# Performance work log

Measured on AMD Instinct MI355X. Metric: run time of the kernel, lower is better.

The kernel has to match this reference:

```python
import jax, jax.numpy as jnp
import numpy as np

N_EMBD = 1024
N_HEAD = 16


def setup_inputs() -> dict:
    key = jax.random.key(0)
    ks = jax.random.split(key, 5)
    C = N_EMBD
    x = jax.random.normal(ks[0], (4, 2048, C), dtype=jnp.float32)
    s = 1.0 / np.sqrt(C)
    W_attn = jax.random.normal(ks[1], (C, 3 * C), dtype=jnp.float32) * s
    b_attn = jnp.zeros((3 * C,), dtype=jnp.float32)
    W_proj = jax.random.normal(ks[2], (C, C), dtype=jnp.float32) * s
    b_proj = jnp.zeros((C,), dtype=jnp.float32)
    return {"x": x, "W_attn": W_attn, "b_attn": b_attn, "W_proj": W_proj, "b_proj": b_proj}


def reference(x, W_attn, b_attn, W_proj, b_proj):
    B, T, C = x.shape
    H = N_HEAD
    D = C // H
    qkv = x @ W_attn + b_attn                      # [B,T,3C]
    q, k, v = jnp.split(qkv, 3, axis=-1)
    # [B,H,T,D]
    q = q.reshape(B, T, H, D).transpose(0, 2, 1, 3)
    k = k.reshape(B, T, H, D).transpose(0, 2, 1, 3)
    v = v.reshape(B, T, H, D).transpose(0, 2, 1, 3)
    scale = 1.0 / jnp.sqrt(jnp.asarray(D, dtype=x.dtype))
    att = jnp.einsum('bhqd,bhkd->bhqk', q, k) * scale   # [B,H,T,T]
    causal = jnp.tril(jnp.ones((T, T), dtype=bool))
    att = jnp.where(causal, att, jnp.finfo(att.dtype).min)
    att = jax.nn.softmax(att, axis=-1)
    y = jnp.einsum('bhqk,bhkd->bhqd', att, v)            # [B,H,T,D]
    y = y.transpose(0, 2, 1, 3).reshape(B, T, C)
    return y @ W_proj + b_proj
```

## Files before the change

### kernel.cpp

```cpp
#include <hip/hip_runtime.h>
#include <type_traits>

typedef __attribute__((ext_vector_type(8))) short short8;
typedef __attribute__((ext_vector_type(8))) unsigned short ushort8;
typedef __attribute__((ext_vector_type(4))) float floatx4;
typedef __attribute__((ext_vector_type(2))) unsigned int uintx2v;

__device__ __forceinline__ unsigned short f2bf(float f) {
    union { float f; unsigned int i; } v;
    v.f = f;
    unsigned int u = v.i;
    unsigned int r = (u + 0x7FFFu + ((u >> 16) & 1u)) >> 16;
    return (unsigned short)r;
}

__device__ __forceinline__ void gload_lds16(const unsigned short* g, unsigned short* lds_base) {
    __builtin_amdgcn_global_load_lds(
        (const __attribute__((address_space(1))) unsigned int*)g,
        (__attribute__((address_space(3))) unsigned int*)lds_base,
        16, 0, 0);
}

__device__ __forceinline__ void pbar() {
    asm volatile("" ::: "memory");
    __builtin_amdgcn_s_barrier();
    asm volatile("" ::: "memory");
}

__global__ __launch_bounds__(256) void cvt_f32_bf16_kernel(
    const float* __restrict__ src, unsigned short* __restrict__ dst, int n8)
{
    int i = blockIdx.x * 256 + threadIdx.x;
    if (i >= n8) return;
    const float4* s = (const float4*)src + (size_t)i * 2;
    float4 a = s[0];
    float4 b = s[1];
    ushort8 r;
    r[0] = f2bf(a.x); r[1] = f2bf(a.y); r[2] = f2bf(a.z); r[3] = f2bf(a.w);
    r[4] = f2bf(b.x); r[5] = f2bf(b.y); r[6] = f2bf(b.z); r[7] = f2bf(b.w);
    *((ushort8*)dst + i) = r;
}

__global__ __launch_bounds__(256) void transpose_cvt_kernel(
    const float* __restrict__ src, unsigned short* __restrict__ dst, int K, int N)
{
    __shared__ float tile[32][33];
    const int tx = threadIdx.x & 31;
    const int ty = threadIdx.x >> 5;
    const int k0 = blockIdx.y * 32, n0 = blockIdx.x * 32;
#pragma unroll
    for (int i = 0; i < 4; ++i)
        tile[ty + i * 8][tx] = src[(size_t)(k0 + ty + i * 8) * N + n0 + tx];
    __syncthreads();
#pragma unroll
    for (int i = 0; i < 4; ++i)
        dst[(size_t)(n0 + ty + i * 8) * K + k0 + tx] = f2bf(tile[tx][ty + i * 8]);
}

template <int MODE, typename OutT>
__global__ __launch_bounds__(256) void gemm128_kernel(
    const unsigned short* __restrict__ A,
    const unsigned short* __restrict__ Bt,
    const float* __restrict__ bias,
    OutT* __restrict__ C,
    unsigned short* __restrict__ Qo,
    unsigned short* __restrict__ Ko,
    unsigned short* __restrict__ Vto,
    int M, int N, int K)
{
    __shared__ __align__(16) unsigned short As[2][128 * 32];
    __shared__ __align__(16) unsigned short Bs[2][128 * 32];

    const int tid  = threadIdx.x;
    const int lane = tid & 63;
    const int w    = tid >> 6;
    const int wm   = w & 1;
    const int wn   = w >> 1;
    const int quad = lane >> 4;
    const int l16  = lane & 15;

    const int m0 = blockIdx.y * 128;
    const int n0 = blockIdx.x * 128;

    floatx4 acc[4][4];
#pragma unroll
    for (int i = 0; i < 4; ++i)
#pragma unroll
        for (int j = 0; j < 4; ++j) acc[i][j] = (floatx4)0.0f;

    const int r0 = tid >> 2;
    const int kc = (((tid & 3) ^ ((tid >> 3) & 3)) << 3);
    const unsigned short* Ag = A  + (size_t)(m0 + r0) * K + kc;
    const unsigned short* Bg = Bt + (size_t)(n0 + r0) * K + kc;

    const int sw = ((quad ^ ((l16 >> 1) & 3)) << 3);

    const int nt = K >> 5;

#define STAGE(buf, t)                                                          \
    do {                                                                       \
        const int kk = (t) << 5;                                               \
        gload_lds16(Ag + kk,                    &As[buf][w * 512]);            \
        gload_lds16(Ag + (size_t)64 * K + kk,   &As[buf][w * 512 + 2048]);     \
        gload_lds16(Bg + kk,                    &Bs[buf][w * 512]);            \
        gload_lds16(Bg + (size_t)64 * K + kk,   &Bs[buf][w * 512 + 2048]);     \
    } while (0)

    STAGE(0, 0);

    for (int t = 0; t < nt; ++t) {
        const int b = t & 1;
        if (t + 1 < nt) {
            STAGE(b ^ 1, t + 1);
            asm volatile("s_waitcnt vmcnt(4)" ::: "memory");
        } else {
            asm volatile("s_waitcnt vmcnt(0)" ::: "memory");
        }
        pbar();

        short8 a[4], bb[4];
#pragma unroll
        for (int mi = 0; mi < 4; ++mi)
            a[mi] = *(const short8*)&As[b][(wm * 64 + mi * 16 + l16) * 32 + sw];
#pragma unroll
        for (int ni = 0; ni < 4; ++ni)
            bb[ni] = *(const short8*)&Bs[b][(wn * 64 + ni * 16 + l16) * 32 + sw];
#pragma unroll
        for (int mi = 0; mi < 4; ++mi)
#pragma unroll
            for (int ni = 0; ni < 4; ++ni)
                acc[mi][ni] = __builtin_amdgcn_mfma_f32_16x16x32_bf16(a[mi], bb[ni], acc[mi][ni], 0, 0, 0);
        pbar();
    }
#undef STAGE

#pragma unroll
    for (int ni = 0; ni < 4; ++ni) {
        const int n = n0 + wn * 64 + ni * 16 + l16;
        const float bval = bias[n];
        const int seg = n >> 10;
        const int nl  = n & 1023;
#pragma unroll
        for (int mi = 0; mi < 4; ++mi) {
            if constexpr (MODE == 0) {
#pragma unroll
                for (int r = 0; r < 4; ++r) {
                    const int m = m0 + wm * 64 + mi * 16 + (quad << 2) + r;
                    const float val = acc[mi][ni][r] + bval;
                    if constexpr (std::is_same<OutT, unsigned short>::value)
                        C[(size_t)m * N + n] = f2bf(val);
                    else
                        C[(size_t)m * N + n] = val;
                }
            } else {
                if (seg < 2) {
                    unsigned short* P = (seg == 0) ? Qo : Ko;
#pragma unroll
                    for (int r = 0; r < 4; ++r) {
                        const int m = m0 + wm * 64 + mi * 16 + (quad << 2) + r;
                        P[(size_t)m * 1024 + nl] = f2bf(acc[mi][ni][r] + bval);
                    }
                } else {
                    const int mb = m0 + wm * 64 + mi * 16 + (quad << 2);
                    const int bbk = mb >> 11, t0 = mb & 2047;
                    unsigned int lo = (unsigned int)f2bf(acc[mi][ni][0] + bval) |
                                      ((unsigned int)f2bf(acc[mi][ni][1] + bval) << 16);
                    unsigned int hi = (unsigned int)f2bf(acc[mi][ni][2] + bval) |
                                      ((unsigned int)f2bf(acc[mi][ni][3] + bval) << 16);
                    uint2 pv; pv.x = lo; pv.y = hi;
                    *(uint2*)(Vto + ((size_t)bbk * 1024 + nl) * 2048 + t0) = pv;
                }
            }
        }
    }
}

__global__ __launch_bounds__(256, 6) void attn_kernel(
    const unsigned short* __restrict__ Q,
    const unsigned short* __restrict__ Kq,
    const unsigned short* __restrict__ Vt,
    unsigned short* __restrict__ Y)
{
    const int T = 2048;

    int idx = blockIdx.x;
    int qt  = 31 - (idx >> 6);
    int bh  = idx & 63;
    int b   = bh >> 4;
    int h   = bh & 15;

    const int tid  = threadIdx.x;
    const int lane = tid & 63;
    const int w    = tid >> 6;
    const int quad = lane >> 4;
    const int l16  = lane & 15;

    __shared__ __align__(16) unsigned short Ks2[8 * 64 * 8];
    __shared__ __align__(16) unsigned short Vs2[8 * 64 * 8];

    const unsigned short* qp =
        Q + (size_t)(b * T + qt * 64 + (w << 4) + l16) * 1024 + h * 64;
    short8 qf0 = *(const short8*)(qp + (quad << 3));
    short8 qf1 = *(const short8*)(qp + 32 + (quad << 3));

    float l_run = 0.0f;
    floatx4 o[4];
#pragma unroll
    for (int ns = 0; ns < 4; ++ns) o[ns] = (floatx4)0.0f;

    const unsigned short* kg0p = Kq + (size_t)(b * T + lane) * 1024 + h * 64 + (w) * 8;
    const unsigned short* kg1p = Kq + (size_t)(b * T + lane) * 1024 + h * 64 + (w + 4) * 8;
    const unsigned short* vg0p = Vt + ((size_t)(b * 1024 + h * 64 + lane)) * 2048 + (w) * 8;
    const unsigned short* vg1p = Vt + ((size_t)(b * 1024 + h * 64 + lane)) * 2048 + (w + 4) * 8;

    const int qg_local = (w << 4) + l16;

    const float SC2 = 0.18033688011112042f;
    const float MB2 = -17.312340490667562f;

    const int ktiles = qt + 1;
    for (int kt = 0; kt < ktiles; ++kt) {
        const int key0 = kt << 6;
        __syncthreads();
        gload_lds16(kg0p + (size_t)key0 * 1024, Ks2 + (w) * 512);
        gload_lds16(kg1p + (size_t)key0 * 1024, Ks2 + (w + 4) * 512);
        gload_lds16(vg0p + key0, Vs2 + (w) * 512);
        gload_lds16(vg1p + key0, Vs2 + (w + 4) * 512);
        __syncthreads();

        floatx4 s[4];
#pragma unroll
        for (int ks = 0; ks < 4; ++ks) {
            s[ks] = (floatx4)0.0f;
            short8 kf0 = *(const short8*)&Ks2[((0 * 4 + quad) * 64 + ks * 16 + l16) * 8];
            short8 kf1 = *(const short8*)&Ks2[((1 * 4 + quad) * 64 + ks * 16 + l16) * 8];
            s[ks] = __builtin_amdgcn_mfma_f32_16x16x32_bf16(kf0, qf0, s[ks], 0, 0, 0);
            s[ks] = __builtin_amdgcn_mfma_f32_16x16x32_bf16(kf1, qf1, s[ks], 0, 0, 0);
        }

        unsigned int plo[4], phi[4];
        if (kt < qt) {
#pragma unroll
            for (int ks = 0; ks < 4; ++ks) {
                float pv0 = __builtin_amdgcn_exp2f(fmaf(s[ks][0], SC2, MB2));
                float pv1 = __builtin_amdgcn_exp2f(fmaf(s[ks][1], SC2, MB2));
                float pv2 = __builtin_amdgcn_exp2f(fmaf(s[ks][2], SC2, MB2));
                float pv3 = __builtin_amdgcn_exp2f(fmaf(s[ks][3], SC2, MB2));
                l_run += (pv0 + pv1) + (pv2 + pv3);
                asm("v_cvt_pk_bf16_f32 %0, %1, %2" : "=v"(plo[ks]) : "v"(pv0), "v"(pv1));
                asm("v_cvt_pk_bf16_f32 %0, %1, %2" : "=v"(phi[ks]) : "v"(pv2), "v"(pv3));
            }
        } else {
            const int kq4 = quad << 2;
#pragma unroll
            for (int ks = 0; ks < 4; ++ks) {
                const int kb = (ks << 4) + kq4;
                float a0 = (kb + 0 <= qg_local) ? fmaf(s[ks][0], SC2, MB2) : -100000.0f;
                float a1 = (kb + 1 <= qg_local) ? fmaf(s[ks][1], SC2, MB2) : -100000.0f;
                float a2 = (kb + 2 <= qg_local) ? fmaf(s[ks][2], SC2, MB2) : -100000.0f;
                float a3 = (kb + 3 <= qg_local) ? fmaf(s[ks][3], SC2, MB2) : -100000.0f;
                float pv0 = __builtin_amdgcn_exp2f(a0);
                float pv1 = __builtin_amdgcn_exp2f(a1);
                float pv2 = __builtin_amdgcn_exp2f(a2);
                float pv3 = __builtin_amdgcn_exp2f(a3);
                l_run += (pv0 + pv1) + (pv2 + pv3);
                asm("v_cvt_pk_bf16_f32 %0, %1, %2" : "=v"(plo[ks]) : "v"(pv0), "v"(pv1));
                asm("v_cvt_pk_bf16_f32 %0, %1, %2" : "=v"(phi[ks]) : "v"(pv2), "v"(pv3));
            }
        }

        uintx2v t0 = __builtin_amdgcn_permlane32_swap(plo[0], plo[1], false, false);
        uintx2v u0 = __builtin_amdgcn_permlane16_swap(t0[0], t0[1], false, false);
        uintx2v t1 = __builtin_amdgcn_permlane32_swap(phi[0], phi[1], false, false);
        uintx2v u1 = __builtin_amdgcn_permlane16_swap(t1[0], t1[1], false, false);
        uintx2v t2 = __builtin_amdgcn_permlane32_swap(plo[2], plo[3], false, false);
        uintx2v u2 = __builtin_amdgcn_permlane16_swap(t2[0], t2[1], false, false);
        uintx2v t3 = __builtin_amdgcn_permlane32_swap(phi[2], phi[3], false, false);
        uintx2v u3 = __builtin_amdgcn_permlane16_swap(t3[0], t3[1], false, false);

        union { unsigned int d[4]; short8 v; } fa, fb;
        fa.d[0] = u0[0]; fa.d[1] = u1[0]; fa.d[2] = u0[1]; fa.d[3] = u1[1];
        fb.d[0] = u2[0]; fb.d[1] = u3[0]; fb.d[2] = u2[1]; fb.d[3] = u3[1];
        const short8 pf0 = fa.v;
        const short8 pf1 = fb.v;

#pragma unroll
        for (int ns = 0; ns < 4; ++ns) {
            short8 vf0 = *(const short8*)&Vs2[((0 * 4 + quad) * 64 + ns * 16 + l16) * 8];
            short8 vf1 = *(const short8*)&Vs2[((1 * 4 + quad) * 64 + ns * 16 + l16) * 8];
            o[ns] = __builtin_amdgcn_mfma_f32_16x16x32_bf16(pf0, vf0, o[ns], 0, 0, 0);
            o[ns] = __builtin_amdgcn_mfma_f32_16x16x32_bf16(pf1, vf1, o[ns], 0, 0, 0);
        }
    }

    float ssum = l_run;
    ssum += __shfl_xor(ssum, 16, 64);
    ssum += __shfl_xor(ssum, 32, 64);
    const float linv = 1.0f / ssum;
    float li[4];
#pragma unroll
    for (int r = 0; r < 4; ++r) li[r] = __shfl(linv, (quad << 2) + r, 64);

#pragma unroll
    for (int ns = 0; ns < 4; ++ns) {
        int d = (ns << 4) + l16;
#pragma unroll
        for (int r = 0; r < 4; ++r) {
            int t = qt * 64 + (w << 4) + (quad << 2) + r;
            Y[(size_t)(b * T + t) * 1024 + h * 64 + d] = f2bf(o[ns][r] * li[r]);
        }
    }
}

extern "C" void kernel_launch(void* const* d_in, const int* in_sizes, int n_in,
                              void* d_out, int out_size, void* d_ws, size_t ws_size,
                              hipStream_t stream) {
    const float* x  = (const float*)d_in[0];
    const float* Wa = (const float*)d_in[1];
    const float* ba = (const float*)d_in[2];
    const float* Wp = (const float*)d_in[3];
    const float* bp = (const float*)d_in[4];
    float* out = (float*)d_out;

    const size_t NX = (size_t)8192 * 1024;

    unsigned short* Qb  = (unsigned short*)d_ws;
    unsigned short* Kb  = Qb  + NX;
    unsigned short* Vtb = Kb  + NX;
    unsigned short* Yb  = Vtb + NX;
    unsigned short* xb  = Yb  + NX;
    unsigned short* Wat = xb  + NX;
    unsigned short* Wpt = Wat + (size_t)3072 * 1024;

    cvt_f32_bf16_kernel<<<(int)(NX / 8 / 256), 256, 0, stream>>>(x, xb, (int)(NX / 8));
    transpose_cvt_kernel<<<dim3(3072 / 32, 1024 / 32), 256, 0, stream>>>(Wa, Wat, 1024, 3072);
    transpose_cvt_kernel<<<dim3(1024 / 32, 1024 / 32), 256, 0, stream>>>(Wp, Wpt, 1024, 1024);

    gemm128_kernel<1, unsigned short><<<dim3(3072 / 128, 8192 / 128), 256, 0, stream>>>(
        xb, Wat, ba, (unsigned short*)nullptr, Qb, Kb, Vtb, 8192, 3072, 1024);

    attn_kernel<<<4 * 16 * (2048 / 64), 256, 0, stream>>>(Qb, Kb, Vtb, Yb);

    gemm128_kernel<0, float><<<dim3(1024 / 128, 8192 / 128), 256, 0, stream>>>(
        Yb, Wpt, bp, out, nullptr, nullptr, nullptr, 8192, 1024, 1024);
}
```

Baseline: 265.6 us.

## Process 128-query tiles per attention block with two 16-row sub-tiles per wave

Each attention block now covers 128 queries instead of 64, and each wave handles two 16-query sub-tiles that share the same K/V fragments loaded into LDS. This halves the number of K/V tile loads from global memory per query and the barrier count per query. Query tiles are assigned in a reordered pattern to balance the causal workload, and waves skip key tiles that lie entirely past their queries. The launch-bounds occupancy hint drops from 6 to 4 to allow the doubled accumulator registers, and the grid halves to 1024 blocks, which gives less parallelism to spread across CUs.

```diff
diff --git a/kernel.cpp b/kernel.cpp
--- a/kernel.cpp
+++ b/kernel.cpp
@@ -175,7 +175,57 @@
     }
 }
 
-__global__ __launch_bounds__(256, 6) void attn_kernel(
+__device__ __forceinline__ void softmax_pack(
+    const floatx4* s, bool masked, int key0, int qg, int kq4,
+    float& l_run, short8& pf0o, short8& pf1o)
+{
+    const float SC2 = 0.18033688011112042f;
+    const float MB2 = -17.312340490667562f;
+    unsigned int plo[4], phi[4];
+    if (!masked) {
+#pragma unroll
+        for (int ks = 0; ks < 4; ++ks) {
+            float pv0 = __builtin_amdgcn_exp2f(fmaf(s[ks][0], SC2, MB2));
+            float pv1 = __builtin_amdgcn_exp2f(fmaf(s[ks][1], SC2, MB2));
+            float pv2 = __builtin_amdgcn_exp2f(fmaf(s[ks][2], SC2, MB2));
+            float pv3 = __builtin_amdgcn_exp2f(fmaf(s[ks][3], SC2, MB2));
+            l_run += (pv0 + pv1) + (pv2 + pv3);
+            asm("v_cvt_pk_bf16_f32 %0, %1, %2" : "=v"(plo[ks]) : "v"(pv0), "v"(pv1));
+            asm("v_cvt_pk_bf16_f32 %0, %1, %2" : "=v"(phi[ks]) : "v"(pv2), "v"(pv3));
+        }
+    } else {
+#pragma unroll
+        for (int ks = 0; ks < 4; ++ks) {
+            const int kb = key0 + (ks << 4) + kq4;
+            float a0 = (kb + 0 <= qg) ? fmaf(s[ks][0], SC2, MB2) : -100000.0f;
+            float a1 = (kb + 1 <= qg) ? fmaf(s[ks][1], SC2, MB2) : -100000.0f;
+            float a2 = (kb + 2 <= qg) ? fmaf(s[ks][2], SC2, MB2) : -100000.0f;
+            float a3 = (kb + 3 <= qg) ? fmaf(s[ks][3], SC2, MB2) : -100000.0f;
+            float pv0 = __builtin_amdgcn_exp2f(a0);
+            float pv1 = __builtin_amdgcn_exp2f(a1);
+            float pv2 = __builtin_amdgcn_exp2f(a2);
+            float pv3 = __builtin_amdgcn_exp2f(a3);
+            l_run += (pv0 + pv1) + (pv2 + pv3);
+            asm("v_cvt_pk_bf16_f32 %0, %1, %2" : "=v"(plo[ks]) : "v"(pv0), "v"(pv1));
+            asm("v_cvt_pk_bf16_f32 %0, %1, %2" : "=v"(phi[ks]) : "v"(pv2), "v"(pv3));
+        }
+    }
+    uintx2v t0 = __builtin_amdgcn_permlane32_swap(plo[0], plo[1], false, false);
+    uintx2v u0 = __builtin_amdgcn_permlane16_swap(t0[0], t0[1], false, false);
+    uintx2v t1 = __builtin_amdgcn_permlane32_swap(phi[0], phi[1], false, false);
+    uintx2v u1 = __builtin_amdgcn_permlane16_swap(t1[0], t1[1], false, false);
+    uintx2v t2 = __builtin_amdgcn_permlane32_swap(plo[2], plo[3], false, false);
+    uintx2v u2 = __builtin_amdgcn_permlane16_swap(t2[0], t2[1], false, false);
+    uintx2v t3 = __builtin_amdgcn_permlane32_swap(phi[2], phi[3], false, false);
+    uintx2v u3 = __builtin_amdgcn_permlane16_swap(t3[0], t3[1], false, false);
+    union { unsigned int d[4]; short8 v; } fa, fb;
+    fa.d[0] = u0[0]; fa.d[1] = u1[0]; fa.d[2] = u0[1]; fa.d[3] = u1[1];
+    fb.d[0] = u2[0]; fb.d[1] = u3[0]; fb.d[2] = u2[1]; fb.d[3] = u3[1];
+    pf0o = fa.v;
+    pf1o = fb.v;
+}
+
+__global__ __launch_bounds__(256, 4) void attn_kernel(
     const unsigned short* __restrict__ Q,
     const unsigned short* __restrict__ Kq,
     const unsigned short* __restrict__ Vt,
@@ -184,7 +234,9 @@
     const int T = 2048;
 
     int idx = blockIdx.x;
-    int qt  = 31 - (idx >> 6);
+    int g   = idx >> 6;
+    int qtp = (g & 4) ? ((g & 8) ? (g - 8) : (g - 4))
+                      : ((g & 8) ? (19 - g) : (15 - g));
     int bh  = idx & 63;
     int b   = bh >> 4;
     int h   = bh & 15;
@@ -198,27 +250,30 @@
     __shared__ __align__(16) unsigned short Ks2[8 * 64 * 8];
     __shared__ __align__(16) unsigned short Vs2[8 * 64 * 8];
 
-    const unsigned short* qp =
-        Q + (size_t)(b * T + qt * 64 + (w << 4) + l16) * 1024 + h * 64;
-    short8 qf0 = *(const short8*)(qp + (quad << 3));
-    short8 qf1 = *(const short8*)(qp + 32 + (quad << 3));
-
-    float l_run = 0.0f;
-    floatx4 o[4];
-#pragma unroll
-    for (int ns = 0; ns < 4; ++ns) o[ns] = (floatx4)0.0f;
+    const int qb = qtp * 128 + (w << 5);
+
+    const unsigned short* qpa = Q + (size_t)(b * T + qb + l16) * 1024 + h * 64;
+    const unsigned short* qpb = qpa + (size_t)16 * 1024;
+    short8 qfa0 = *(const short8*)(qpa + (quad << 3));
+    short8 qfa1 = *(const short8*)(qpa + 32 + (quad << 3));
+    short8 qfb0 = *(const short8*)(qpb + (quad << 3));
+    short8 qfb1 = *(const short8*)(qpb + 32 + (quad << 3));
+
+    float lra = 0.0f, lrb = 0.0f;
+    floatx4 oa[4], ob[4];
+#pragma unroll
+    for (int ns = 0; ns < 4; ++ns) { oa[ns] = (floatx4)0.0f; ob[ns] = (floatx4)0.0f; }
 
     const unsigned short* kg0p = Kq + (size_t)(b * T + lane) * 1024 + h * 64 + (w) * 8;
     const unsigned short* kg1p = Kq + (size_t)(b * T + lane) * 1024 + h * 64 + (w + 4) * 8;
     const unsigned short* vg0p = Vt + ((size_t)(b * 1024 + h * 64 + lane)) * 2048 + (w) * 8;
     const unsigned short* vg1p = Vt + ((size_t)(b * 1024 + h * 64 + lane)) * 2048 + (w + 4) * 8;
 
-    const int qg_local = (w << 4) + l16;
-
-    const float SC2 = 0.18033688011112042f;
-    const float MB2 = -17.312340490667562f;
-
-    const int ktiles = qt + 1;
+    const int qa_g = qb + l16;
+    const int qb_g = qb + 16 + l16;
+    const int kq4  = quad << 2;
+
+    const int ktiles = 2 * qtp + 2;
     for (int kt = 0; kt < ktiles; ++kt) {
         const int key0 = kt << 6;
         __syncthreads();
@@ -228,86 +283,59 @@
         gload_lds16(vg1p + key0, Vs2 + (w + 4) * 512);
         __syncthreads();
 
-        floatx4 s[4];
-#pragma unroll
-        for (int ks = 0; ks < 4; ++ks) {
-            s[ks] = (floatx4)0.0f;
-            short8 kf0 = *(const short8*)&Ks2[((0 * 4 + quad) * 64 + ks * 16 + l16) * 8];
-            short8 kf1 = *(const short8*)&Ks2[((1 * 4 + quad) * 64 + ks * 16 + l16) * 8];
-            s[ks] = __builtin_amdgcn_mfma_f32_16x16x32_bf16(kf0, qf0, s[ks], 0, 0, 0);
-            s[ks] = __builtin_amdgcn_mfma_f32_16x16x32_bf16(kf1, qf1, s[ks], 0, 0, 0);
-        }
-
-        unsigned int plo[4], phi[4];
-        if (kt < qt) {
+        if (key0 <= qb + 31) {
+            floatx4 sa[4], sb[4];
 #pragma unroll
             for (int ks = 0; ks < 4; ++ks) {
-                float pv0 = __builtin_amdgcn_exp2f(fmaf(s[ks][0], SC2, MB2));
-                float pv1 = __builtin_amdgcn_exp2f(fmaf(s[ks][1], SC2, MB2));
-                float pv2 = __builtin_amdgcn_exp2f(fmaf(s[ks][2], SC2, MB2));
-                float pv3 = __builtin_amdgcn_exp2f(fmaf(s[ks][3], SC2, MB2));
-                l_run += (pv0 + pv1) + (pv2 + pv3);
-                asm("v_cvt_pk_bf16_f32 %0, %1, %2" : "=v"(plo[ks]) : "v"(pv0), "v"(pv1));
-                asm("v_cvt_pk_bf16_f32 %0, %1, %2" : "=v"(phi[ks]) : "v"(pv2), "v"(pv3));
+                short8 kf0 = *(const short8*)&Ks2[((0 * 4 + quad) * 64 + ks * 16 + l16) * 8];
+                short8 kf1 = *(const short8*)&Ks2[((1 * 4 + quad) * 64 + ks * 16 + l16) * 8];
+                sa[ks] = __builtin_amdgcn_mfma_f32_16x16x32_bf16(kf0, qfa0, (floatx4)0.0f, 0, 0, 0);
+                sa[ks] = __builtin_amdgcn_mfma_f32_16x16x32_bf16(kf1, qfa1, sa[ks], 0, 0, 0);
+                sb[ks] = __builtin_amdgcn_mfma_f32_16x16x32_bf16(kf0, qfb0, (floatx4)0.0f, 0, 0, 0);
+                sb[ks] = __builtin_amdgcn_mfma_f32_16x16x32_bf16(kf1, qfb1, sb[ks], 0, 0, 0);
             }
-        } else {
-            const int kq4 = quad << 2;
-#pragma unroll
-            for (int ks = 0; ks < 4; ++ks) {
-                const int kb = (ks << 4) + kq4;
-                float a0 = (kb + 0 <= qg_local) ? fmaf(s[ks][0], SC2, MB2) : -100000.0f;
-                float a1 = (kb + 1 <= qg_local) ? fmaf(s[ks][1], SC2, MB2) : -100000.0f;
-                float a2 = (kb + 2 <= qg_local) ? fmaf(s[ks][2], SC2, MB2) : -100000.0f;
-                float a3 = (kb + 3 <= qg_local) ? fmaf(s[ks][3], SC2, MB2) : -100000.0f;
-                float pv0 = __builtin_amdgcn_exp2f(a0);
-                float pv1 = __builtin_amdgcn_exp2f(a1);
-                float pv2 = __builtin_amdgcn_exp2f(a2);
-                float pv3 = __builtin_amdgcn_exp2f(a3);
-                l_run += (pv0 + pv1) + (pv2 + pv3);
-                asm("v_cvt_pk_bf16_f32 %0, %1, %2" : "=v"(plo[ks]) : "v"(pv0), "v"(pv1));
-                asm("v_cvt_pk_bf16_f32 %0, %1, %2" : "=v"(phi[ks]) : "v"(pv2), "v"(pv3));
+
+            const bool masked = (key0 + 64 > qb);
+            short8 pa0, pa1, pb0, pb1;
+            softmax_pack(sa, masked, key0, qa_g, kq4, lra, pa0, pa1);
+            softmax_pack(sb, masked, key0, qb_g, kq4, lrb, pb0, pb1);
+
+#pragma unroll
+            for (int ns = 0; ns < 4; ++ns) {
+                short8 vf0 = *(const short8*)&Vs2[((0 * 4 + quad) * 64 + ns * 16 + l16) * 8];
+                short8 vf1 = *(const short8*)&Vs2[((1 * 4 + quad) * 64 + ns * 16 + l16) * 8];
+                oa[ns] = __builtin_amdgcn_mfma_f32_16x16x32_bf16(pa0, vf0, oa[ns], 0, 0, 0);
+                oa[ns] = __builtin_amdgcn_mfma_f32_16x16x32_bf16(pa1, vf1, oa[ns], 0, 0, 0);
+                ob[ns] = __builtin_amdgcn_mfma_f32_16x16x32_bf16(pb0, vf0, ob[ns], 0, 0, 0);
+                ob[ns] = __builtin_amdgcn_mfma_f32_16x16x32_bf16(pb1, vf1, ob[ns], 0, 0, 0);
             }
         }
-
-        uintx2v t0 = __builtin_amdgcn_permlane32_swap(plo[0], plo[1], false, false);
-        uintx2v u0 = __builtin_amdgcn_permlane16_swap(t0[0], t0[1], false, false);
-        uintx2v t1 = __builtin_amdgcn_permlane32_swap(phi[0], phi[1], false, false);
-        uintx2v u1 = __builtin_amdgcn_permlane16_swap(t1[0], t1[1], false, false);
-        uintx2v t2 = __builtin_amdgcn_permlane32_swap(plo[2], plo[3], false, false);
-        uintx2v u2 = __builtin_amdgcn_permlane16_swap(t2[0], t2[1], false, false);
-        uintx2v t3 = __builtin_amdgcn_permlane32_swap(phi[2], phi[3], false, false);
-        uintx2v u3 = __builtin_amdgcn_permlane16_swap(t3[0], t3[1], false, false);
-
-        union { unsigned int d[4]; short8 v; } fa, fb;
-        fa.d[0] = u0[0]; fa.d[1] = u1[0]; fa.d[2] = u0[1]; fa.d[3] = u1[1];
-        fb.d[0] = u2[0]; fb.d[1] = u3[0]; fb.d[2] = u2[1]; fb.d[3] = u3[1];
-        const short8 pf0 = fa.v;
-        const short8 pf1 = fb.v;
-
-#pragma unroll
-        for (int ns = 0; ns < 4; ++ns) {
-            short8 vf0 = *(const short8*)&Vs2[((0 * 4 + quad) * 64 + ns * 16 + l16) * 8];
-            short8 vf1 = *(const short8*)&Vs2[((1 * 4 + quad) * 64 + ns * 16 + l16) * 8];
-            o[ns] = __builtin_amdgcn_mfma_f32_16x16x32_bf16(pf0, vf0, o[ns], 0, 0, 0);
-            o[ns] = __builtin_amdgcn_mfma_f32_16x16x32_bf16(pf1, vf1, o[ns], 0, 0, 0);
-        }
-    }
-
-    float ssum = l_run;
-    ssum += __shfl_xor(ssum, 16, 64);
-    ssum += __shfl_xor(ssum, 32, 64);
-    const float linv = 1.0f / ssum;
-    float li[4];
-#pragma unroll
-    for (int r = 0; r < 4; ++r) li[r] = __shfl(linv, (quad << 2) + r, 64);
+    }
+
+    float sa_ = lra;
+    sa_ += __shfl_xor(sa_, 16, 64);
+    sa_ += __shfl_xor(sa_, 32, 64);
+    const float lia = 1.0f / sa_;
+    float sb_ = lrb;
+    sb_ += __shfl_xor(sb_, 16, 64);
+    sb_ += __shfl_xor(sb_, 32, 64);
+    const float lib = 1.0f / sb_;
+
+    float la[4], lb[4];
+#pragma unroll
+    for (int r = 0; r < 4; ++r) {
+        la[r] = __shfl(lia, (quad << 2) + r, 64);
+        lb[r] = __shfl(lib, (quad << 2) + r, 64);
+    }
 
 #pragma unroll
     for (int ns = 0; ns < 4; ++ns) {
         int d = (ns << 4) + l16;
 #pragma unroll
         for (int r = 0; r < 4; ++r) {
-            int t = qt * 64 + (w << 4) + (quad << 2) + r;
-            Y[(size_t)(b * T + t) * 1024 + h * 64 + d] = f2bf(o[ns][r] * li[r]);
+            int ta = qb + (quad << 2) + r;
+            Y[(size_t)(b * T + ta) * 1024 + h * 64 + d]        = f2bf(oa[ns][r] * la[r]);
+            Y[(size_t)(b * T + ta + 16) * 1024 + h * 64 + d]   = f2bf(ob[ns][r] * lb[r]);
         }
     }
 }
@@ -339,7 +367,7 @@
     gemm128_kernel<1, unsigned short><<<dim3(3072 / 128, 8192 / 128), 256, 0, stream>>>(
         xb, Wat, ba, (unsigned short*)nullptr, Qb, Kb, Vtb, 8192, 3072, 1024);
 
-    attn_kernel<<<4 * 16 * (2048 / 64), 256, 0, stream>>>(Qb, Kb, Vtb, Yb);
+    attn_kernel<<<4 * 16 * (2048 / 128), 256, 0, stream>>>(Qb, Kb, Vtb, Yb);
 
     gemm128_kernel<0, float><<<dim3(1024 / 128, 8192 / 128), 256, 0, stream>>>(
         Yb, Wpt, bp, out, nullptr, nullptr, nullptr, 8192, 1024, 1024);
```

Result: faster. 246.3 us (-7.3%).
